# Kernel tuning notes

Measured on AMD Instinct MI355X. Metric: run time of the kernel, lower is better.

## Reference

```python
import jax, jax.numpy as jnp
import numpy as np

N_NODES = 20000
N_EDGES = 320000
HIDDEN = 64
HEADS = 4
D_INNER = 256
NEG_SLOPE = 0.2
BN_EPS = 1e-5


def setup_inputs() -> dict:
    key = jax.random.key(0)
    ks = jax.random.split(key, 8)
    s = 1.0 / np.sqrt(HIDDEN)
    return {
        "x": jax.random.normal(ks[0], (N_NODES, HIDDEN), jnp.float32),
        "edge_index": jax.random.randint(ks[1], (2, N_EDGES), 0, N_NODES, jnp.int64),
        "W_l": jax.random.normal(ks[2], (HIDDEN, HEADS * HIDDEN), jnp.float32) * s,
        "b_l": jnp.zeros((HEADS * HIDDEN,), jnp.float32),
        "W_r": jax.random.normal(ks[3], (HIDDEN, HEADS * HIDDEN), jnp.float32) * s,
        "b_r": jnp.zeros((HEADS * HIDDEN,), jnp.float32),
        "att": jax.random.normal(ks[4], (HEADS, HIDDEN), jnp.float32) * s,
        "bias_gat": jnp.zeros((HIDDEN,), jnp.float32),
        "gamma1": jnp.ones((HIDDEN,), jnp.float32),
        "beta1": jnp.zeros((HIDDEN,), jnp.float32),
        "W1": jax.random.normal(ks[5], (HIDDEN, D_INNER), jnp.float32) * s,
        "b1": jnp.zeros((D_INNER,), jnp.float32),
        "W2": jax.random.normal(ks[6], (D_INNER, HIDDEN), jnp.float32) / np.sqrt(D_INNER),
        "b2": jnp.zeros((HIDDEN,), jnp.float32),
        "gamma2": jnp.ones((HIDDEN,), jnp.float32),
        "beta2": jnp.zeros((HIDDEN,), jnp.float32),
    }


def _batch_norm(x, gamma, beta):
    # training-mode BatchNorm1d over the node axis (biased variance, as torch)
    mu = x.mean(0)
    var = jnp.mean((x - mu) ** 2, axis=0)
    return (x - mu) * jax.lax.rsqrt(var + BN_EPS) * gamma + beta


def _gatv2(x, edge_index, W_l, b_l, W_r, b_r, att, bias_gat):
    N = x.shape[0]
    H, C = att.shape
    src, dst = edge_index[0], edge_index[1]  # j (source), i (target)
    xl = (x @ W_l + b_l).reshape(N, H, C)  # messages (x_j side)
    xr = (x @ W_r + b_r).reshape(N, H, C)  # target (x_i side)
    # GATv2 dynamic attention: a^T LeakyReLU(x_i + x_j), per head
    e = jax.nn.leaky_relu(xl[src] + xr[dst], NEG_SLOPE)  # [E, H, C]
    score = jnp.einsum("ehc,hc->eh", e, att)  # [E, H]
    # segment softmax over incoming edges of each target node
    m = jax.ops.segment_max(score, dst, num_segments=N)  # [N, H]
    ex = jnp.exp(score - m[dst])
    denom = jax.ops.segment_sum(ex, dst, num_segments=N)  # [N, H]
    alpha = ex / jnp.maximum(denom[dst], 1e-16)  # [E, H]
    out = jax.ops.segment_sum(alpha[:, :, None] * xl[src], dst, num_segments=N)  # [N, H, C]
    return out.mean(axis=1) + bias_gat  # concat=False -> mean over heads


def reference(x, edge_index, W_l, b_l, W_r, b_r, att, bias_gat,
              gamma1, beta1, W1, b1, W2, b2, gamma2, beta2):
    x2 = _gatv2(x, edge_index, W_l, b_l, W_r, b_r, att, bias_gat)
    x = x + x2  # dropout is identity in eval
    x = _batch_norm(x, gamma1, beta1)
    ff = jax.nn.relu(x @ W1 + b1) @ W2 + b2
    x = x + ff
    x = _batch_norm(x, gamma2, beta2)
    return x
```

## Files before the change

### kernel.cpp

```cpp
#include <hip/hip_runtime.h>
#include <hip/hip_bf16.h>
#include <math.h>

#define N_NODES 20000
#define N_EDGES 320000
#define HIDDEN 64
#define HEADS 4
#define HC 256
#define D_INNER 256
#define NEG_SLOPE 0.2f
#define BN_EPS 1e-5f
#define MAXDEG 64
#define NZERO (N_NODES + 2048)

typedef __attribute__((ext_vector_type(8))) short short8;
typedef __attribute__((ext_vector_type(4))) float f32x4;

__device__ __forceinline__ float lrelu(float v) { return v >= 0.f ? v : NEG_SLOPE * v; }
__device__ __forceinline__ float bf2f(unsigned short u) {
    unsigned x = ((unsigned)u) << 16;
    return __uint_as_float(x);
}
__device__ __forceinline__ unsigned short f2bf(float f) {
    __hip_bfloat16 b = __float2bfloat16(f);
    return *reinterpret_cast<unsigned short*>(&b);
}

__global__ __launch_bounds__(256) void k_wprep(const float* __restrict__ W1, const float* __restrict__ W2,
                                               const float* __restrict__ Wl, const float* __restrict__ Wr,
                                               unsigned short* __restrict__ W1tb, unsigned short* __restrict__ W2tb,
                                               unsigned short* __restrict__ Wlrtb,
                                               int* __restrict__ zbuf) {
    int idx = blockIdx.x * 256 + threadIdx.x;
    if (idx < NZERO) zbuf[idx] = 0;
    if (idx < 16384) {
        int k = idx >> 8, n = idx & 255;
        W1tb[n * 64 + k] = f2bf(W1[idx]);
    } else if (idx < 32768) {
        int j = idx - 16384;
        int k = j >> 6, n = j & 63;
        W2tb[n * 256 + k] = f2bf(W2[j]);
    } else if (idx < 49152) {
        int j = idx - 32768;
        int k = j >> 8, n = j & 255;
        Wlrtb[n * 64 + k] = f2bf(Wl[j]);
    } else {
        int j = idx - 49152;
        int k = j >> 8, n = j & 255;
        Wlrtb[16384 + n * 64 + k] = f2bf(Wr[j]);
    }
}

__global__ __launch_bounds__(256) void k_linm(const float* __restrict__ x,
                                              const unsigned short* __restrict__ Wlrtb,
                                              const float* __restrict__ bl, const float* __restrict__ br,
                                              unsigned short* __restrict__ xlb, unsigned short* __restrict__ xrb) {
    __shared__ unsigned short sW[16384];
    int t = threadIdx.x;
    int w = t >> 6, lane = t & 63;
    int l15 = lane & 15, lg = lane >> 4;
    int side = blockIdx.x & 1;
    int row0 = (blockIdx.x >> 1) * 64;
    const float* bias = side ? br : bl;
    unsigned short* dst = side ? xrb : xlb;
    {
        const short8* src = (const short8*)(Wlrtb + side * 16384);
#pragma unroll
        for (int it = 0; it < 8; ++it) {
            int i = it * 256 + t;
            int n = i >> 3, c = i & 7;
            *(short8*)((char*)sW + n * 128 + ((c * 16) ^ ((n & 7) << 4))) = src[i];
        }
    }
    short8 af[4][2];
#pragma unroll
    for (int mt = 0; mt < 4; ++mt) {
        int gm = row0 + mt * 16 + l15;
        bool valid = gm < N_NODES;
#pragma unroll
        for (int kk = 0; kk < 2; ++kk) {
            int k0 = kk * 32 + lg * 8;
            float4 v0 = {0.f,0.f,0.f,0.f}, v1 = {0.f,0.f,0.f,0.f};
            if (valid) {
                v0 = *(const float4*)(x + (size_t)gm * 64 + k0);
                v1 = *(const float4*)(x + (size_t)gm * 64 + k0 + 4);
            }
            short8 f;
            f[0] = (short)f2bf(v0.x); f[1] = (short)f2bf(v0.y);
            f[2] = (short)f2bf(v0.z); f[3] = (short)f2bf(v0.w);
            f[4] = (short)f2bf(v1.x); f[5] = (short)f2bf(v1.y);
            f[6] = (short)f2bf(v1.z); f[7] = (short)f2bf(v1.w);
            af[mt][kk] = f;
        }
    }
    float bv[4];
#pragma unroll
    for (int nt = 0; nt < 4; ++nt) bv[nt] = bias[w * 64 + nt * 16 + l15];
    __syncthreads();
    f32x4 zero4 = {0.f, 0.f, 0.f, 0.f};
    f32x4 acc[4][4];
#pragma unroll
    for (int mt = 0; mt < 4; ++mt)
#pragma unroll
        for (int nt = 0; nt < 4; ++nt) acc[mt][nt] = zero4;
#pragma unroll
    for (int kk = 0; kk < 2; ++kk) {
        int kb = kk * 64 + lg * 16;
        short8 bf[4];
#pragma unroll
        for (int nt = 0; nt < 4; ++nt) {
            int n = w * 64 + nt * 16 + l15;
            bf[nt] = *(const short8*)((const char*)sW + n * 128 + (kb ^ ((n & 7) << 4)));
        }
#pragma unroll
        for (int mt = 0; mt < 4; ++mt)
#pragma unroll
            for (int nt = 0; nt < 4; ++nt)
                acc[mt][nt] = __builtin_amdgcn_mfma_f32_16x16x32_bf16(af[mt][kk], bf[nt], acc[mt][nt], 0, 0, 0);
    }
#pragma unroll
    for (int mt = 0; mt < 4; ++mt)
#pragma unroll
        for (int nt = 0; nt < 4; ++nt) {
            int n = w * 64 + nt * 16 + l15;
#pragma unroll
            for (int r = 0; r < 4; ++r) {
                int gm = row0 + mt * 16 + lg * 4 + r;
                if (gm < N_NODES)
                    dst[(size_t)gm * 256 + n] = f2bf(acc[mt][nt][r] + bv[nt]);
            }
        }
}

__global__ __launch_bounds__(256) void k_fill(const int* __restrict__ ei,
                                              int* __restrict__ cursor, int* __restrict__ perm) {
    int e = blockIdx.x * 256 + threadIdx.x;
    int dst = ei[N_EDGES + e];
    int slot = atomicAdd(&cursor[dst], 1);
    perm[dst * MAXDEG + slot] = ei[e];
}

__global__ __launch_bounds__(256) void k_gat(const unsigned short* __restrict__ xlb,
                                             const unsigned short* __restrict__ xrb,
                                             const float* __restrict__ att,
                                             const int* __restrict__ perm,
                                             const int* __restrict__ cnt,
                                             const float* __restrict__ x,
                                             const float* __restrict__ bias,
                                             float* __restrict__ y1,
                                             float* __restrict__ gsum, float* __restrict__ gsq) {
    __shared__ float ps[4][64], pq[4][64];
    int wv = threadIdx.x >> 6;
    int node = blockIdx.x * 4 + wv;
    int lane = threadIdx.x & 63;
    ushort4 xru = *reinterpret_cast<const ushort4*>(xrb + (size_t)node * 256 + lane * 4);
    float4 xrv = {bf2f(xru.x), bf2f(xru.y), bf2f(xru.z), bf2f(xru.w)};
    float4 atv = *reinterpret_cast<const float4*>(att + lane * 4);
    int deg = cnt[node];
    const int* ep = perm + (size_t)node * MAXDEG;
    const ushort4* xl4 = reinterpret_cast<const ushort4*>(xlb);
    float m = -INFINITY, d = 0.f;
    float4 acc = {0.f, 0.f, 0.f, 0.f};
    if (deg > 0) {
        ushort4 uv = xl4[(size_t)ep[0] * 64 + lane];
        for (int j = 0; j < deg; ++j) {
            int jn = (j + 1 < deg) ? j + 1 : j;
            ushort4 uv_n = xl4[(size_t)ep[jn] * 64 + lane];
            float4 xf;
            xf.x = bf2f(uv.x); xf.y = bf2f(uv.y); xf.z = bf2f(uv.z); xf.w = bf2f(uv.w);
            float p = lrelu(xf.x + xrv.x) * atv.x
                    + lrelu(xf.y + xrv.y) * atv.y
                    + lrelu(xf.z + xrv.z) * atv.z
                    + lrelu(xf.w + xrv.w) * atv.w;
            p += __shfl_xor(p, 1);
            p += __shfl_xor(p, 2);
            p += __shfl_xor(p, 4);
            p += __shfl_xor(p, 8);
            float delta = p - m;
            if (delta > 8.f) {
                float sc = __expf(-delta);
                acc.x *= sc; acc.y *= sc; acc.z *= sc; acc.w *= sc;
                d *= sc; m = p; delta = 0.f;
            }
            float w = __expf(delta);
            d += w;
            acc.x += w * xf.x; acc.y += w * xf.y; acc.z += w * xf.z; acc.w += w * xf.w;
            uv = uv_n;
        }
    }
    float inv = 1.f / fmaxf(d, 1e-16f);
    float4 v;
    v.x = acc.x * inv; v.y = acc.y * inv; v.z = acc.z * inv; v.w = acc.w * inv;
    v.x += __shfl_xor(v.x, 16); v.y += __shfl_xor(v.y, 16);
    v.z += __shfl_xor(v.z, 16); v.w += __shfl_xor(v.w, 16);
    v.x += __shfl_xor(v.x, 32); v.y += __shfl_xor(v.y, 32);
    v.z += __shfl_xor(v.z, 32); v.w += __shfl_xor(v.w, 32);
    if (lane < 16) {
        float4 xv = *reinterpret_cast<const float4*>(x + (size_t)node * 64 + lane * 4);
        float4 bv = *reinterpret_cast<const float4*>(bias + lane * 4);
        float4 y;
        y.x = xv.x + 0.25f * v.x + bv.x;
        y.y = xv.y + 0.25f * v.y + bv.y;
        y.z = xv.z + 0.25f * v.z + bv.z;
        y.w = xv.w + 0.25f * v.w + bv.w;
        *reinterpret_cast<float4*>(y1 + (size_t)node * 64 + lane * 4) = y;
        int c = lane * 4;
        ps[wv][c+0] = y.x; ps[wv][c+1] = y.y; ps[wv][c+2] = y.z; ps[wv][c+3] = y.w;
        pq[wv][c+0] = y.x*y.x; pq[wv][c+1] = y.y*y.y; pq[wv][c+2] = y.z*y.z; pq[wv][c+3] = y.w*y.w;
    }
    __syncthreads();
    int t = threadIdx.x;
    if (t < 64) {
        int r = blockIdx.x & 7;
        atomicAdd(&gsum[r * 64 + t], ps[0][t] + ps[1][t] + ps[2][t] + ps[3][t]);
        atomicAdd(&gsq [r * 64 + t], pq[0][t] + pq[1][t] + pq[2][t] + pq[3][t]);
    }
}

__global__ __launch_bounds__(256) void k_ffn(const float* __restrict__ y1,
                                             const float* __restrict__ s1, const float* __restrict__ q1,
                                             const float* __restrict__ gamma1, const float* __restrict__ beta1,
                                             const unsigned short* __restrict__ W1tb, const float* __restrict__ b1,
                                             const unsigned short* __restrict__ W2tb, const float* __restrict__ b2,
                                             float* __restrict__ out,
                                             float* __restrict__ gsum2, float* __restrict__ gsq2) {
    __shared__ unsigned short sW[16384];
    __shared__ unsigned short sH[16384];
    __shared__ __align__(16) float sA1[64], sC1[64];
    int t = threadIdx.x;
    int w = t >> 6, lane = t & 63;
    int l15 = lane & 15, lg = lane >> 4;
    int blk = blockIdx.x;

    {
        const short8* src = (const short8*)W1tb;
#pragma unroll
        for (int it = 0; it < 8; ++it) {
            int i = it * 256 + t;
            int n = i >> 3, c = i & 7;
            *(short8*)((char*)sW + n * 128 + ((c * 16) ^ ((n & 7) << 4))) = src[i];
        }
    }
    if (t < 64) {
        float s = 0.f, q = 0.f;
#pragma unroll
        for (int r = 0; r < 8; ++r) { s += s1[r * 64 + t]; q += q1[r * 64 + t]; }
        float mu = s * (1.0f / N_NODES);
        float var = fmaxf(q * (1.0f / N_NODES) - mu * mu, 0.f);
        float av = gamma1[t] * rsqrtf(var + BN_EPS);
        sA1[t] = av; sC1[t] = beta1[t] - mu * av;
    }
    __syncthreads();

    float4 a1k[2][2], c1k[2][2];
#pragma unroll
    for (int kk = 0; kk < 2; ++kk) {
        int k0 = kk * 32 + lg * 8;
        a1k[kk][0] = *(const float4*)(sA1 + k0); a1k[kk][1] = *(const float4*)(sA1 + k0 + 4);
        c1k[kk][0] = *(const float4*)(sC1 + k0); c1k[kk][1] = *(const float4*)(sC1 + k0 + 4);
    }
    short8 af[4][2];
#pragma unroll
    for (int mt = 0; mt < 4; ++mt) {
        int gm = blk * 64 + mt * 16 + l15;
        bool valid = gm < N_NODES;
#pragma unroll
        for (int kk = 0; kk < 2; ++kk) {
            int k0 = kk * 32 + lg * 8;
            float4 v0 = {0.f,0.f,0.f,0.f}, v1 = {0.f,0.f,0.f,0.f};
            if (valid) {
                v0 = *(const float4*)(y1 + (size_t)gm * 64 + k0);
                v1 = *(const float4*)(y1 + (size_t)gm * 64 + k0 + 4);
            }
            short8 f;
            f[0] = (short)f2bf(fmaf(a1k[kk][0].x, v0.x, c1k[kk][0].x));
            f[1] = (short)f2bf(fmaf(a1k[kk][0].y, v0.y, c1k[kk][0].y));
            f[2] = (short)f2bf(fmaf(a1k[kk][0].z, v0.z, c1k[kk][0].z));
            f[3] = (short)f2bf(fmaf(a1k[kk][0].w, v0.w, c1k[kk][0].w));
            f[4] = (short)f2bf(fmaf(a1k[kk][1].x, v1.x, c1k[kk][1].x));
            f[5] = (short)f2bf(fmaf(a1k[kk][1].y, v1.y, c1k[kk][1].y));
            f[6] = (short)f2bf(fmaf(a1k[kk][1].z, v1.z, c1k[kk][1].z));
            f[7] = (short)f2bf(fmaf(a1k[kk][1].w, v1.w, c1k[kk][1].w));
            af[mt][kk] = f;
        }
    }
    float b1v[4];
#pragma unroll
    for (int nt = 0; nt < 4; ++nt) b1v[nt] = b1[w * 64 + nt * 16 + l15];

    f32x4 zero4 = {0.f, 0.f, 0.f, 0.f};
    f32x4 acc[4][4];
#pragma unroll
    for (int mt = 0; mt < 4; ++mt)
#pragma unroll
        for (int nt = 0; nt < 4; ++nt) acc[mt][nt] = zero4;
#pragma unroll
    for (int kk = 0; kk < 2; ++kk) {
        int kb = kk * 64 + lg * 16;
        short8 bf[4];
#pragma unroll
        for (int nt = 0; nt < 4; ++nt) {
            int n = w * 64 + nt * 16 + l15;
            bf[nt] = *(const short8*)((const char*)sW + n * 128 + (kb ^ ((n & 7) << 4)));
        }
#pragma unroll
        for (int mt = 0; mt < 4; ++mt)
#pragma unroll
            for (int nt = 0; nt < 4; ++nt)
                acc[mt][nt] = __builtin_amdgcn_mfma_f32_16x16x32_bf16(af[mt][kk], bf[nt], acc[mt][nt], 0, 0, 0);
    }
    __syncthreads();

#pragma unroll
    for (int mt = 0; mt < 4; ++mt)
#pragma unroll
        for (int nt = 0; nt < 4; ++nt) {
            int n = w * 64 + nt * 16 + l15;
#pragma unroll
            for (int r = 0; r < 4; ++r) {
                int m = mt * 16 + lg * 4 + r;
                float h = fmaxf(acc[mt][nt][r] + b1v[nt], 0.f);
                *(unsigned short*)((char*)sH + m * 512 + ((n * 2) ^ ((m & 7) << 4))) = f2bf(h);
            }
        }
    {
        const short8* src = (const short8*)W2tb;
#pragma unroll
        for (int it = 0; it < 8; ++it) {
            int i = it * 256 + t;
            int n = i >> 5, c = i & 31;
            *(short8*)((char*)sW + n * 512 + ((c * 16) ^ ((n & 7) << 4))) = src[i];
        }
    }
    __syncthreads();

    f32x4 acc2[4];
#pragma unroll
    for (int nt = 0; nt < 4; ++nt) acc2[nt] = zero4;
#pragma unroll
    for (int kk = 0; kk < 8; ++kk) {
        int kb = kk * 64 + lg * 16;
        int m = w * 16 + l15;
        short8 a2 = *(const short8*)((const char*)sH + m * 512 + (kb ^ ((m & 7) << 4)));
#pragma unroll
        for (int nt = 0; nt < 4; ++nt) {
            int n = nt * 16 + l15;
            short8 b2f = *(const short8*)((const char*)sW + n * 512 + (kb ^ ((n & 7) << 4)));
            acc2[nt] = __builtin_amdgcn_mfma_f32_16x16x32_bf16(a2, b2f, acc2[nt], 0, 0, 0);
        }
    }

    float b2v[4], a1n[4], c1n[4], ssum[4] = {0.f,0.f,0.f,0.f}, ssq[4] = {0.f,0.f,0.f,0.f};
#pragma unroll
    for (int nt = 0; nt < 4; ++nt) {
        int n = nt * 16 + l15;
        b2v[nt] = b2[n]; a1n[nt] = sA1[n]; c1n[nt] = sC1[n];
    }
#pragma unroll
    for (int nt = 0; nt < 4; ++nt) {
        int n = nt * 16 + l15;
#pragma unroll
        for (int r = 0; r < 4; ++r) {
            int gm = blk * 64 + w * 16 + lg * 4 + r;
            if (gm < N_NODES) {
                float v = acc2[nt][r] + b2v[nt] + fmaf(a1n[nt], y1[(size_t)gm * 64 + n], c1n[nt]);
                out[(size_t)gm * 64 + n] = v;
                ssum[nt] += v; ssq[nt] += v * v;
            }
        }
    }
    __syncthreads();
    float* fs = (float*)sW;
#pragma unroll
    for (int nt = 0; nt < 4; ++nt) {
        float ss = ssum[nt], qq = ssq[nt];
        ss += __shfl_xor(ss, 16); ss += __shfl_xor(ss, 32);
        qq += __shfl_xor(qq, 16); qq += __shfl_xor(qq, 32);
        if (lg == 0) {
            int n = nt * 16 + l15;
            fs[w * 64 + n] = ss;
            fs[256 + w * 64 + n] = qq;
        }
    }
    __syncthreads();
    if (t < 64) {
        int r = blk & 7;
        atomicAdd(&gsum2[r * 64 + t], fs[t] + fs[64 + t] + fs[128 + t] + fs[192 + t]);
        atomicAdd(&gsq2 [r * 64 + t], fs[256 + t] + fs[320 + t] + fs[384 + t] + fs[448 + t]);
    }
}

__global__ __launch_bounds__(256) void k_apply(float* __restrict__ out,
                                               const float* __restrict__ s2, const float* __restrict__ q2,
                                               const float* __restrict__ gamma2, const float* __restrict__ beta2) {
    __shared__ float sA[64], sC[64];
    int t = threadIdx.x;
    if (t < 64) {
        float s = 0.f, q = 0.f;
#pragma unroll
        for (int r = 0; r < 8; ++r) { s += s2[r * 64 + t]; q += q2[r * 64 + t]; }
        float mu = s * (1.0f / N_NODES);
        float var = fmaxf(q * (1.0f / N_NODES) - mu * mu, 0.f);
        float av = gamma2[t] * rsqrtf(var + BN_EPS);
        sA[t] = av; sC[t] = beta2[t] - mu * av;
    }
    __syncthreads();
    int idx = blockIdx.x * 256 + t;
    int ch = idx & 63;
    out[idx] = sA[ch] * out[idx] + sC[ch];
}

extern "C" void kernel_launch(void* const* d_in, const int* in_sizes, int n_in,
                              void* d_out, int out_size, void* d_ws, size_t ws_size,
                              hipStream_t stream) {
    const float* x        = (const float*)d_in[0];
    const int*   ei       = (const int*)d_in[1];
    const float* Wl       = (const float*)d_in[2];
    const float* bl       = (const float*)d_in[3];
    const float* Wr       = (const float*)d_in[4];
    const float* br       = (const float*)d_in[5];
    const float* att      = (const float*)d_in[6];
    const float* bias_gat = (const float*)d_in[7];
    const float* gamma1   = (const float*)d_in[8];
    const float* beta1    = (const float*)d_in[9];
    const float* W1       = (const float*)d_in[10];
    const float* b1       = (const float*)d_in[11];
    const float* W2       = (const float*)d_in[12];
    const float* b2       = (const float*)d_in[13];
    const float* gamma2   = (const float*)d_in[14];
    const float* beta2    = (const float*)d_in[15];
    float* out = (float*)d_out;

    char* ws = (char*)d_ws;
    unsigned short* xlb = (unsigned short*)ws;
    unsigned short* xrb = xlb + (size_t)N_NODES * HC;
    float* y1    = (float*)(xrb + (size_t)N_NODES * HC);
    int*   perm  = (int*)(y1 + (size_t)N_NODES * HIDDEN);
    int*   cursor= perm + (size_t)N_NODES * MAXDEG;
    float* stats = (float*)(cursor + N_NODES);
    unsigned short* W1tb  = (unsigned short*)(stats + 2048);
    unsigned short* W2tb  = W1tb + 16384;
    unsigned short* Wlrtb = W2tb + 16384;

    k_wprep<<<256, 256, 0, stream>>>(W1, W2, Wl, Wr, W1tb, W2tb, Wlrtb, cursor);
    k_linm <<<((N_NODES + 63) / 64) * 2, 256, 0, stream>>>(x, Wlrtb, bl, br, xlb, xrb);
    k_fill <<<N_EDGES / 256, 256, 0, stream>>>(ei, cursor, perm);
    k_gat  <<<N_NODES / 4, 256, 0, stream>>>(xlb, xrb, att, perm, cursor, x, bias_gat, y1,
                                             stats + 0, stats + 512);
    k_ffn  <<<(N_NODES + 63) / 64, 256, 0, stream>>>(y1, stats + 0, stats + 512, gamma1, beta1,
                                                     W1tb, b1, W2tb, b2, out,
                                                     stats + 1024, stats + 1536);
    k_apply<<<N_NODES * HIDDEN / 256, 256, 0, stream>>>(out, stats + 1024, stats + 1536, gamma2, beta2);
}
```

Measured before the change: 106.5 us.

## Fuse edge fill into linear kernel and restructure GAT aggregation per half-wave

The CSR fill kernel is merged into the linear-projection kernel as extra blocks, removing one launch. The GAT kernel now handles one node per 32-lane half-wave, with 8 bf16 channels per lane loaded as uint4. LeakyReLU is rewritten as 0.6v+0.4|v|, and the online max-rescaling of the softmax is dropped in favour of plain exp. The half-waves iterate to the larger degree of the pair and mask out the extra steps. Without the max subtraction, exp can overflow if attention scores ever get large, and the pair-wise loop does wasted work when the two degrees differ.

New measurement: 91.12 us. -14.4%, faster.

```diff
diff --git a/kernel.cpp b/kernel.cpp
--- a/kernel.cpp
+++ b/kernel.cpp
@@ -12,11 +12,12 @@
 #define BN_EPS 1e-5f
 #define MAXDEG 64
 #define NZERO (N_NODES + 2048)
+#define NB_LIN 626
+#define NB_FILL 1250
 
 typedef __attribute__((ext_vector_type(8))) short short8;
 typedef __attribute__((ext_vector_type(4))) float f32x4;
 
-__device__ __forceinline__ float lrelu(float v) { return v >= 0.f ? v : NEG_SLOPE * v; }
 __device__ __forceinline__ float bf2f(unsigned short u) {
     unsigned x = ((unsigned)u) << 16;
     return __uint_as_float(x);
@@ -24,15 +25,22 @@
 __device__ __forceinline__ unsigned short f2bf(float f) {
     __hip_bfloat16 b = __float2bfloat16(f);
     return *reinterpret_cast<unsigned short*>(&b);
+}
+__device__ __forceinline__ void cvt8(uint4 u, float* f) {
+    f[0] = __uint_as_float(u.x << 16); f[1] = __uint_as_float(u.x & 0xFFFF0000u);
+    f[2] = __uint_as_float(u.y << 16); f[3] = __uint_as_float(u.y & 0xFFFF0000u);
+    f[4] = __uint_as_float(u.z << 16); f[5] = __uint_as_float(u.z & 0xFFFF0000u);
+    f[6] = __uint_as_float(u.w << 16); f[7] = __uint_as_float(u.w & 0xFFFF0000u);
 }
 
 __global__ __launch_bounds__(256) void k_wprep(const float* __restrict__ W1, const float* __restrict__ W2,
                                                const float* __restrict__ Wl, const float* __restrict__ Wr,
                                                unsigned short* __restrict__ W1tb, unsigned short* __restrict__ W2tb,
                                                unsigned short* __restrict__ Wlrtb,
-                                               int* __restrict__ zbuf) {
+                                               int* __restrict__ zbuf, int* __restrict__ perm) {
     int idx = blockIdx.x * 256 + threadIdx.x;
     if (idx < NZERO) zbuf[idx] = 0;
+    if (idx < N_NODES) perm[idx * MAXDEG] = 0;
     if (idx < 16384) {
         int k = idx >> 8, n = idx & 255;
         W1tb[n * 64 + k] = f2bf(W1[idx]);
@@ -51,12 +59,21 @@
     }
 }
 
-__global__ __launch_bounds__(256) void k_linm(const float* __restrict__ x,
+__global__ __launch_bounds__(256) void k_prep(const float* __restrict__ x,
                                               const unsigned short* __restrict__ Wlrtb,
                                               const float* __restrict__ bl, const float* __restrict__ br,
-                                              unsigned short* __restrict__ xlb, unsigned short* __restrict__ xrb) {
+                                              unsigned short* __restrict__ xlb, unsigned short* __restrict__ xrb,
+                                              const int* __restrict__ ei,
+                                              int* __restrict__ cursor, int* __restrict__ perm) {
     __shared__ unsigned short sW[16384];
     int t = threadIdx.x;
+    if (blockIdx.x >= NB_LIN) {
+        int e = (blockIdx.x - NB_LIN) * 256 + t;
+        int ed = ei[N_EDGES + e];
+        int slot = atomicAdd(&cursor[ed], 1);
+        perm[ed * MAXDEG + slot] = ei[e];
+        return;
+    }
     int w = t >> 6, lane = t & 63;
     int l15 = lane & 15, lg = lane >> 4;
     int side = blockIdx.x & 1;
@@ -132,14 +149,6 @@
         }
 }
 
-__global__ __launch_bounds__(256) void k_fill(const int* __restrict__ ei,
-                                              int* __restrict__ cursor, int* __restrict__ perm) {
-    int e = blockIdx.x * 256 + threadIdx.x;
-    int dst = ei[N_EDGES + e];
-    int slot = atomicAdd(&cursor[dst], 1);
-    perm[dst * MAXDEG + slot] = ei[e];
-}
-
 __global__ __launch_bounds__(256) void k_gat(const unsigned short* __restrict__ xlb,
                                              const unsigned short* __restrict__ xrb,
                                              const float* __restrict__ att,
@@ -149,71 +158,85 @@
                                              const float* __restrict__ bias,
                                              float* __restrict__ y1,
                                              float* __restrict__ gsum, float* __restrict__ gsq) {
-    __shared__ float ps[4][64], pq[4][64];
-    int wv = threadIdx.x >> 6;
-    int node = blockIdx.x * 4 + wv;
-    int lane = threadIdx.x & 63;
-    ushort4 xru = *reinterpret_cast<const ushort4*>(xrb + (size_t)node * 256 + lane * 4);
-    float4 xrv = {bf2f(xru.x), bf2f(xru.y), bf2f(xru.z), bf2f(xru.w)};
-    float4 atv = *reinterpret_cast<const float4*>(att + lane * 4);
+    __shared__ float ps[8][64], pq[8][64];
+    int t = threadIdx.x;
+    int hw = t >> 5, l = t & 31;
+    int node = blockIdx.x * 8 + hw;
+    const uint4* xl4 = (const uint4*)xlb;
+    uint4 xru = ((const uint4*)xrb)[(size_t)node * 32 + l];
+    float xr[8]; cvt8(xru, xr);
+    float at[8];
+    *(float4*)(at)     = *(const float4*)(att + l * 8);
+    *(float4*)(at + 4) = *(const float4*)(att + l * 8 + 4);
     int deg = cnt[node];
+    int mdeg = max(deg, __shfl_xor(deg, 32));
     const int* ep = perm + (size_t)node * MAXDEG;
-    const ushort4* xl4 = reinterpret_cast<const ushort4*>(xlb);
-    float m = -INFINITY, d = 0.f;
-    float4 acc = {0.f, 0.f, 0.f, 0.f};
-    if (deg > 0) {
-        ushort4 uv = xl4[(size_t)ep[0] * 64 + lane];
-        for (int j = 0; j < deg; ++j) {
-            int jn = (j + 1 < deg) ? j + 1 : j;
-            ushort4 uv_n = xl4[(size_t)ep[jn] * 64 + lane];
-            float4 xf;
-            xf.x = bf2f(uv.x); xf.y = bf2f(uv.y); xf.z = bf2f(uv.z); xf.w = bf2f(uv.w);
-            float p = lrelu(xf.x + xrv.x) * atv.x
-                    + lrelu(xf.y + xrv.y) * atv.y
-                    + lrelu(xf.z + xrv.z) * atv.z
-                    + lrelu(xf.w + xrv.w) * atv.w;
-            p += __shfl_xor(p, 1);
-            p += __shfl_xor(p, 2);
-            p += __shfl_xor(p, 4);
-            p += __shfl_xor(p, 8);
-            float delta = p - m;
-            if (delta > 8.f) {
-                float sc = __expf(-delta);
-                acc.x *= sc; acc.y *= sc; acc.z *= sc; acc.w *= sc;
-                d *= sc; m = p; delta = 0.f;
-            }
-            float w = __expf(delta);
-            d += w;
-            acc.x += w * xf.x; acc.y += w * xf.y; acc.z += w * xf.z; acc.w += w * xf.w;
-            uv = uv_n;
-        }
+    float d = 0.f;
+    float acc[8] = {0.f,0.f,0.f,0.f,0.f,0.f,0.f,0.f};
+    uint4 uv = xl4[(size_t)ep[0] * 32 + l];
+    for (int j = 0; j < mdeg; ++j) {
+        int jn = (j + 1 < deg) ? (j + 1) : ((deg > 0) ? (deg - 1) : 0);
+        uint4 un = xl4[(size_t)ep[jn] * 32 + l];
+        float xl[8]; cvt8(uv, xl);
+        float v[8];
+        float sv0 = 0.f, sv1 = 0.f, sa0 = 0.f, sa1 = 0.f;
+#pragma unroll
+        for (int i = 0; i < 8; i += 2) {
+            v[i] = xl[i] + xr[i];
+            v[i+1] = xl[i+1] + xr[i+1];
+            sv0 = fmaf(at[i], v[i], sv0);
+            sa0 = fmaf(at[i], fabsf(v[i]), sa0);
+            sv1 = fmaf(at[i+1], v[i+1], sv1);
+            sa1 = fmaf(at[i+1], fabsf(v[i+1]), sa1);
+        }
+        float s = 0.6f * (sv0 + sv1) + 0.4f * (sa0 + sa1);
+        s += __shfl_xor(s, 1);
+        s += __shfl_xor(s, 2);
+        s += __shfl_xor(s, 4);
+        float w = (j < deg) ? __expf(s) : 0.f;
+        d += w;
+#pragma unroll
+        for (int i = 0; i < 8; ++i) acc[i] = fmaf(w, xl[i], acc[i]);
+        uv = un;
     }
     float inv = 1.f / fmaxf(d, 1e-16f);
-    float4 v;
-    v.x = acc.x * inv; v.y = acc.y * inv; v.z = acc.z * inv; v.w = acc.w * inv;
-    v.x += __shfl_xor(v.x, 16); v.y += __shfl_xor(v.y, 16);
-    v.z += __shfl_xor(v.z, 16); v.w += __shfl_xor(v.w, 16);
-    v.x += __shfl_xor(v.x, 32); v.y += __shfl_xor(v.y, 32);
-    v.z += __shfl_xor(v.z, 32); v.w += __shfl_xor(v.w, 32);
-    if (lane < 16) {
-        float4 xv = *reinterpret_cast<const float4*>(x + (size_t)node * 64 + lane * 4);
-        float4 bv = *reinterpret_cast<const float4*>(bias + lane * 4);
-        float4 y;
-        y.x = xv.x + 0.25f * v.x + bv.x;
-        y.y = xv.y + 0.25f * v.y + bv.y;
-        y.z = xv.z + 0.25f * v.z + bv.z;
-        y.w = xv.w + 0.25f * v.w + bv.w;
-        *reinterpret_cast<float4*>(y1 + (size_t)node * 64 + lane * 4) = y;
-        int c = lane * 4;
-        ps[wv][c+0] = y.x; ps[wv][c+1] = y.y; ps[wv][c+2] = y.z; ps[wv][c+3] = y.w;
-        pq[wv][c+0] = y.x*y.x; pq[wv][c+1] = y.y*y.y; pq[wv][c+2] = y.z*y.z; pq[wv][c+3] = y.w*y.w;
-    }
-    __syncthreads();
-    int t = threadIdx.x;
+#pragma unroll
+    for (int i = 0; i < 8; ++i) {
+        float v2 = acc[i] * inv;
+        v2 += __shfl_xor(v2, 8);
+        v2 += __shfl_xor(v2, 16);
+        acc[i] = v2;
+    }
+    if (l < 8) {
+        float4 xv0 = *(const float4*)(x + (size_t)node * 64 + l * 8);
+        float4 xv1 = *(const float4*)(x + (size_t)node * 64 + l * 8 + 4);
+        float4 bv0 = *(const float4*)(bias + l * 8);
+        float4 bv1 = *(const float4*)(bias + l * 8 + 4);
+        float4 y0, y1v;
+        y0.x = xv0.x + 0.25f * acc[0] + bv0.x;
+        y0.y = xv0.y + 0.25f * acc[1] + bv0.y;
+        y0.z = xv0.z + 0.25f * acc[2] + bv0.z;
+        y0.w = xv0.w + 0.25f * acc[3] + bv0.w;
+        y1v.x = xv1.x + 0.25f * acc[4] + bv1.x;
+        y1v.y = xv1.y + 0.25f * acc[5] + bv1.y;
+        y1v.z = xv1.z + 0.25f * acc[6] + bv1.z;
+        y1v.w = xv1.w + 0.25f * acc[7] + bv1.w;
+        *(float4*)(y1 + (size_t)node * 64 + l * 8) = y0;
+        *(float4*)(y1 + (size_t)node * 64 + l * 8 + 4) = y1v;
+        int c = l * 8;
+        ps[hw][c+0] = y0.x; ps[hw][c+1] = y0.y; ps[hw][c+2] = y0.z; ps[hw][c+3] = y0.w;
+        ps[hw][c+4] = y1v.x; ps[hw][c+5] = y1v.y; ps[hw][c+6] = y1v.z; ps[hw][c+7] = y1v.w;
+        pq[hw][c+0] = y0.x*y0.x; pq[hw][c+1] = y0.y*y0.y; pq[hw][c+2] = y0.z*y0.z; pq[hw][c+3] = y0.w*y0.w;
+        pq[hw][c+4] = y1v.x*y1v.x; pq[hw][c+5] = y1v.y*y1v.y; pq[hw][c+6] = y1v.z*y1v.z; pq[hw][c+7] = y1v.w*y1v.w;
+    }
+    __syncthreads();
     if (t < 64) {
-        int r = blockIdx.x & 7;
-        atomicAdd(&gsum[r * 64 + t], ps[0][t] + ps[1][t] + ps[2][t] + ps[3][t]);
-        atomicAdd(&gsq [r * 64 + t], pq[0][t] + pq[1][t] + pq[2][t] + pq[3][t]);
+        float s = 0.f, q = 0.f;
+#pragma unroll
+        for (int r = 0; r < 8; ++r) { s += ps[r][t]; q += pq[r][t]; }
+        int rb = blockIdx.x & 7;
+        atomicAdd(&gsum[rb * 64 + t], s);
+        atomicAdd(&gsq [rb * 64 + t], q);
     }
 }
 
@@ -442,10 +465,9 @@
     unsigned short* W2tb  = W1tb + 16384;
     unsigned short* Wlrtb = W2tb + 16384;
 
-    k_wprep<<<256, 256, 0, stream>>>(W1, W2, Wl, Wr, W1tb, W2tb, Wlrtb, cursor);
-    k_linm <<<((N_NODES + 63) / 64) * 2, 256, 0, stream>>>(x, Wlrtb, bl, br, xlb, xrb);
-    k_fill <<<N_EDGES / 256, 256, 0, stream>>>(ei, cursor, perm);
-    k_gat  <<<N_NODES / 4, 256, 0, stream>>>(xlb, xrb, att, perm, cursor, x, bias_gat, y1,
+    k_wprep<<<256, 256, 0, stream>>>(W1, W2, Wl, Wr, W1tb, W2tb, Wlrtb, cursor, perm);
+    k_prep <<<NB_LIN + NB_FILL, 256, 0, stream>>>(x, Wlrtb, bl, br, xlb, xrb, ei, cursor, perm);
+    k_gat  <<<N_NODES / 8, 256, 0, stream>>>(xlb, xrb, att, perm, cursor, x, bias_gat, y1,
                                              stats + 0, stats + 512);
     k_ffn  <<<(N_NODES + 63) / 64, 256, 0, stream>>>(y1, stats + 0, stats + 512, gamma1, beta1,
                                                      W1tb, b1, W2tb, b2, out,
```
